# Performance work log

Hardware: AMD Instinct MI355X
Metric: run time of the kernel (lower is better)

The kernel has to match this reference:

```python
import jax, jax.numpy as jnp
import numpy as np

B, N = 1, 50000          # batch (module assumes 1), retrieval library size
VD, AD, OCRD, OD = 768, 768, 768, 384  # vision / audio / ocr / option dims
TOP_K = 25


def _l2norm(x):
    # torch.nn.functional.normalize(p=2, dim=-1) with eps=1e-12
    n = jnp.linalg.norm(x, axis=-1, keepdims=True)
    return x / jnp.maximum(n, 1e-12)


def setup_inputs() -> dict:
    key = jax.random.key(0)
    ks = jax.random.split(key, 8)
    return {
        "v":       jax.random.normal(ks[0], (B, VD), jnp.float32),
        "n_feats": jax.random.normal(ks[1], (B, N, VD), jnp.float32),
        "aud":     jax.random.normal(ks[2], (B, AD), jnp.float32),
        "n_auds":  jax.random.normal(ks[3], (B, N, AD), jnp.float32),
        "ocr":     jax.random.uniform(ks[4], (B, OCRD), jnp.float32),  # positive -> ocr.sum() > 0 branch
        "n_ocrs":  jax.random.normal(ks[5], (B, N, OCRD), jnp.float32),
        "o":       jax.random.normal(ks[6], (B, 3, OD), jnp.float32),
        "n_answ":  jax.random.normal(ks[7], (B, N, OD), jnp.float32),
        # learned temperature params (init zeros, as in torch)
        "temp_vid": jnp.zeros((1,), jnp.float32),
        "temp_aud": jnp.zeros((1,), jnp.float32),
        "temp_ocr": jnp.zeros((1,), jnp.float32),
    }


def _modal_attn(q, k):
    # normalized cosine scores, clipped to [0,1], then softmax over library dim
    s = jnp.einsum("bd,bnd->bn", _l2norm(q), _l2norm(k))
    return jax.nn.softmax(jnp.clip(s, 0.0, 1.0), axis=-1)


def reference(v, n_feats, aud, n_auds, ocr, n_ocrs, o, n_answ,
              temp_vid, temp_aud, temp_ocr):
    # gates (note: aud/ocr gates are multiplied by 0 exactly as in the source)
    vid_gate = jax.nn.sigmoid(temp_vid) * 2.0
    aud_gate = jax.nn.sigmoid(temp_aud) * 0.0
    ocr_gate = jax.nn.sigmoid(temp_ocr) * 0.0

    attention = (_modal_attn(v, n_feats) * vid_gate
                 + _modal_attn(aud, n_auds) * aud_gate
                 + _modal_attn(ocr, n_ocrs) * ocr_gate)  # [B, N]

    # TopKGroup (skip_self=False): keep only top-k entries via scatter mask
    _, idx = jax.lax.top_k(attention, TOP_K)            # [B, K]
    mask = jnp.zeros((attention.shape[-1],), attention.dtype).at[idx[0]].set(1.0)
    attention = attention * mask[None, :]

    # weighted sum of candidate answer embeddings, then dot with 3 options
    oia = jnp.einsum("bn,bnd->bd", attention, n_answ)   # [B, OD]
    scores = jnp.einsum("bd,bkd->bk", oia, o)           # [B, 3]
    return scores
```

## Files before the change

kernel.cpp:

```cpp
#include <hip/hip_runtime.h>
#include <cstdint>
#include <cstddef>

typedef unsigned long long u64;
typedef unsigned int u32;

constexpr int N    = 50000;
constexpr int D    = 768;
constexpr int OD   = 384;
constexpr int TOPK = 25;

constexpr int K1_BLOCKS  = 2048;
constexpr int K1_THREADS = 256;
constexpr int WAVES_TOTAL = K1_BLOCKS * (K1_THREADS / 64);

constexpr int N4    = 12500;
constexpr int BURST = 12;
constexpr int TAIL4 = N4 - BURST * 1024;
constexpr int CAP   = 4096;

constexpr int BINSHIFT = 20;

__global__ __launch_bounds__(K1_THREADS)
void k_scores(const float* __restrict__ v,
              const float* __restrict__ n_feats,
              float* __restrict__ s_out,
              float* __restrict__ part_out)
{
    const int lane  = threadIdx.x & 63;
    const int wib   = threadIdx.x >> 6;
    const int gwave = blockIdx.x * 4 + wib;

    const float4* v4 = reinterpret_cast<const float4*>(v);
    const float4 va = v4[lane];
    const float4 vb = v4[lane + 64];
    const float4 vc = v4[lane + 128];

    float vsq = 0.f;
    vsq = fmaf(va.x, va.x, vsq); vsq = fmaf(va.y, va.y, vsq);
    vsq = fmaf(va.z, va.z, vsq); vsq = fmaf(va.w, va.w, vsq);
    vsq = fmaf(vb.x, vb.x, vsq); vsq = fmaf(vb.y, vb.y, vsq);
    vsq = fmaf(vb.z, vb.z, vsq); vsq = fmaf(vb.w, vb.w, vsq);
    vsq = fmaf(vc.x, vc.x, vsq); vsq = fmaf(vc.y, vc.y, vsq);
    vsq = fmaf(vc.w, vc.w, vsq); vsq = fmaf(vc.z, vc.z, vsq);
    #pragma unroll
    for (int off = 32; off; off >>= 1) vsq += __shfl_xor(vsq, off);
    const float inv_vn = 1.0f / fmaxf(sqrtf(vsq), 1e-12f);

    float esum = 0.f;
    for (int r = 2 * gwave; r < N; r += 2 * WAVES_TOTAL) {
        const float4* f0 = reinterpret_cast<const float4*>(n_feats + (size_t)r * D);
        const float4* f1 = reinterpret_cast<const float4*>(n_feats + (size_t)(r + 1) * D);
        const float4 a0 = f0[lane];
        const float4 a1 = f0[lane + 64];
        const float4 a2 = f0[lane + 128];
        const float4 b0 = f1[lane];
        const float4 b1 = f1[lane + 64];
        const float4 b2 = f1[lane + 128];

        float dA = 0.f, nA = 0.f, dB = 0.f, nB = 0.f;
        dA = fmaf(a0.x, va.x, dA); nA = fmaf(a0.x, a0.x, nA);
        dB = fmaf(b0.x, va.x, dB); nB = fmaf(b0.x, b0.x, nB);
        dA = fmaf(a0.y, va.y, dA); nA = fmaf(a0.y, a0.y, nA);
        dB = fmaf(b0.y, va.y, dB); nB = fmaf(b0.y, b0.y, nB);
        dA = fmaf(a0.z, va.z, dA); nA = fmaf(a0.z, a0.z, nA);
        dB = fmaf(b0.z, va.z, dB); nB = fmaf(b0.z, b0.z, nB);
        dA = fmaf(a0.w, va.w, dA); nA = fmaf(a0.w, a0.w, nA);
        dB = fmaf(b0.w, va.w, dB); nB = fmaf(b0.w, b0.w, nB);
        dA = fmaf(a1.x, vb.x, dA); nA = fmaf(a1.x, a1.x, nA);
        dB = fmaf(b1.x, vb.x, dB); nB = fmaf(b1.x, b1.x, nB);
        dA = fmaf(a1.y, vb.y, dA); nA = fmaf(a1.y, a1.y, nA);
        dB = fmaf(b1.y, vb.y, dB); nB = fmaf(b1.y, b1.y, nB);
        dA = fmaf(a1.z, vb.z, dA); nA = fmaf(a1.z, a1.z, nA);
        dB = fmaf(b1.z, vb.z, dB); nB = fmaf(b1.z, b1.z, nB);
        dA = fmaf(a1.w, vb.w, dA); nA = fmaf(a1.w, a1.w, nA);
        dB = fmaf(b1.w, vb.w, dB); nB = fmaf(b1.w, b1.w, nB);
        dA = fmaf(a2.x, vc.x, dA); nA = fmaf(a2.x, a2.x, nA);
        dB = fmaf(b2.x, vc.x, dB); nB = fmaf(b2.x, b2.x, nB);
        dA = fmaf(a2.y, vc.y, dA); nA = fmaf(a2.y, a2.y, nA);
        dB = fmaf(b2.y, vc.y, dB); nB = fmaf(b2.y, b2.y, nB);
        dA = fmaf(a2.z, vc.z, dA); nA = fmaf(a2.z, a2.z, nA);
        dB = fmaf(b2.z, vc.z, dB); nB = fmaf(b2.z, b2.z, nB);
        dA = fmaf(a2.w, vc.w, dA); nA = fmaf(a2.w, a2.w, nA);
        dB = fmaf(b2.w, vc.w, dB); nB = fmaf(b2.w, b2.w, nB);

        #pragma unroll
        for (int off = 32; off; off >>= 1) {
            dA += __shfl_xor(dA, off);
            nA += __shfl_xor(nA, off);
            dB += __shfl_xor(dB, off);
            nB += __shfl_xor(nB, off);
        }

        float sA = dA * inv_vn / fmaxf(sqrtf(nA), 1e-12f);
        sA = fminf(fmaxf(sA, 0.f), 1.f);
        float sB = dB * inv_vn / fmaxf(sqrtf(nB), 1e-12f);
        sB = fminf(fmaxf(sB, 0.f), 1.f);
        if (lane == 0) {
            float2 sv; sv.x = sA; sv.y = sB;
            *reinterpret_cast<float2*>(s_out + r) = sv;
        }
        esum += expf(sA) + expf(sB);
    }

    __shared__ float wsum[4];
    if (lane == 0) wsum[wib] = esum;
    __syncthreads();
    if (threadIdx.x == 0)
        part_out[blockIdx.x] = (wsum[0] + wsum[1]) + (wsum[2] + wsum[3]);
}

__global__ __launch_bounds__(1024)
void k_finish(const float4* __restrict__ s4,
              const float* __restrict__ part,
              const float* __restrict__ n_answ,
              const float* __restrict__ o,
              const float* __restrict__ temp_vid,
              float* __restrict__ out)
{
    __shared__ u32   hist[1024];
    __shared__ u32   sufb[1024];
    __shared__ float redA[1024], redB[1024], redC[1024];
    __shared__ u64   L[CAP];
    __shared__ u64   Ls[TOPK];
    __shared__ float topw[TOPK];
    __shared__ int   topi[TOPK];
    __shared__ u32   ctrL;
    __shared__ int   b1sh;
    __shared__ float zsh;

    const int tid = threadIdx.x;

    redA[tid] = part[tid] + part[tid + 1024];
    hist[tid] = 0;
    if (tid == 0) { ctrL = 0; b1sh = 0; }
    __syncthreads();
    for (int s = 512; s > 0; s >>= 1) {
        if (tid < s) redA[tid] += redA[tid + s];
        __syncthreads();
    }
    if (tid == 0) zsh = redA[0];

    {
        float4 r[BURST];
        #pragma unroll
        for (int j = 0; j < BURST; ++j) r[j] = s4[tid + j * 1024];
        float4 rt;
        if (tid < TAIL4) rt = s4[BURST * 1024 + tid];

        #pragma unroll
        for (int j = 0; j < BURST; ++j) {
            u32 b;
            b = __float_as_uint(r[j].x); if (b) atomicAdd(&hist[b >> BINSHIFT], 1u);
            b = __float_as_uint(r[j].y); if (b) atomicAdd(&hist[b >> BINSHIFT], 1u);
            b = __float_as_uint(r[j].z); if (b) atomicAdd(&hist[b >> BINSHIFT], 1u);
            b = __float_as_uint(r[j].w); if (b) atomicAdd(&hist[b >> BINSHIFT], 1u);
        }
        if (tid < TAIL4) {
            u32 b;
            b = __float_as_uint(rt.x); if (b) atomicAdd(&hist[b >> BINSHIFT], 1u);
            b = __float_as_uint(rt.y); if (b) atomicAdd(&hist[b >> BINSHIFT], 1u);
            b = __float_as_uint(rt.z); if (b) atomicAdd(&hist[b >> BINSHIFT], 1u);
            b = __float_as_uint(rt.w); if (b) atomicAdd(&hist[b >> BINSHIFT], 1u);
        }
    }
    __syncthreads();

    {
        u32* src = hist;
        u32* dst = sufb;
        for (int s = 1; s < 1024; s <<= 1) {
            dst[tid] = src[tid] + ((tid + s < 1024) ? src[tid + s] : 0u);
            __syncthreads();
            u32* t_ = src; src = dst; dst = t_;
        }
        if (src[tid] >= (u32)TOPK && (tid == 1023 || src[tid + 1] < (u32)TOPK))
            b1sh = tid;
    }
    __syncthreads();
    const int b1 = b1sh;

    {
        float4 r[BURST];
        #pragma unroll
        for (int j = 0; j < BURST; ++j) r[j] = s4[tid + j * 1024];
        float4 rt;
        if (tid < TAIL4) rt = s4[BURST * 1024 + tid];

        #pragma unroll
        for (int j = 0; j < BURST; ++j) {
            const int base = (tid + j * 1024) * 4;
            u32 b;
            b = __float_as_uint(r[j].x);
            if (b && (int)(b >> BINSHIFT) >= b1) { u32 p = atomicAdd(&ctrL, 1u); if (p < CAP) L[p] = ((u64)b << 32) | (u64)(0xFFFFFFFFu - (u32)(base + 0)); }
            b = __float_as_uint(r[j].y);
            if (b && (int)(b >> BINSHIFT) >= b1) { u32 p = atomicAdd(&ctrL, 1u); if (p < CAP) L[p] = ((u64)b << 32) | (u64)(0xFFFFFFFFu - (u32)(base + 1)); }
            b = __float_as_uint(r[j].z);
            if (b && (int)(b >> BINSHIFT) >= b1) { u32 p = atomicAdd(&ctrL, 1u); if (p < CAP) L[p] = ((u64)b << 32) | (u64)(0xFFFFFFFFu - (u32)(base + 2)); }
            b = __float_as_uint(r[j].w);
            if (b && (int)(b >> BINSHIFT) >= b1) { u32 p = atomicAdd(&ctrL, 1u); if (p < CAP) L[p] = ((u64)b << 32) | (u64)(0xFFFFFFFFu - (u32)(base + 3)); }
        }
        if (tid < TAIL4) {
            const int base = (BURST * 1024 + tid) * 4;
            u32 b;
            b = __float_as_uint(rt.x);
            if (b && (int)(b >> BINSHIFT) >= b1) { u32 p = atomicAdd(&ctrL, 1u); if (p < CAP) L[p] = ((u64)b << 32) | (u64)(0xFFFFFFFFu - (u32)(base + 0)); }
            b = __float_as_uint(rt.y);
            if (b && (int)(b >> BINSHIFT) >= b1) { u32 p = atomicAdd(&ctrL, 1u); if (p < CAP) L[p] = ((u64)b << 32) | (u64)(0xFFFFFFFFu - (u32)(base + 1)); }
            b = __float_as_uint(rt.z);
            if (b && (int)(b >> BINSHIFT) >= b1) { u32 p = atomicAdd(&ctrL, 1u); if (p < CAP) L[p] = ((u64)b << 32) | (u64)(0xFFFFFFFFu - (u32)(base + 2)); }
            b = __float_as_uint(rt.w);
            if (b && (int)(b >> BINSHIFT) >= b1) { u32 p = atomicAdd(&ctrL, 1u); if (p < CAP) L[p] = ((u64)b << 32) | (u64)(0xFFFFFFFFu - (u32)(base + 3)); }
        }
    }
    __syncthreads();

    const int nL = (int)((ctrL < (u32)CAP) ? ctrL : (u32)CAP);
    for (int i = tid; i < nL; i += 1024) {
        const u64 ki = L[i];
        int rank = 0;
        for (int j = 0; j < nL; ++j) rank += (L[j] > ki);
        if (rank < TOPK) Ls[rank] = ki;
    }
    __syncthreads();

    if (tid < TOPK) {
        const u64 kk = Ls[tid];
        topw[tid] = expf(__uint_as_float((u32)(kk >> 32)));
        topi[tid] = (int)(0xFFFFFFFFu - (u32)(kk & 0xFFFFFFFFu));
    }
    __syncthreads();

    const float gate  = 2.f / (1.f + expf(-temp_vid[0]));
    const float scale = gate / zsh;
    float oia_ = 0.f;
    if (tid < OD) {
        #pragma unroll
        for (int j = 0; j < TOPK; ++j)
            oia_ = fmaf(topw[j] * scale, n_answ[(size_t)topi[j] * OD + tid], oia_);
    }
    redA[tid] = (tid < OD) ? oia_ * o[0 * OD + tid] : 0.f;
    redB[tid] = (tid < OD) ? oia_ * o[1 * OD + tid] : 0.f;
    redC[tid] = (tid < OD) ? oia_ * o[2 * OD + tid] : 0.f;
    __syncthreads();
    for (int s = 512; s > 0; s >>= 1) {
        if (tid < s) {
            redA[tid] += redA[tid + s];
            redB[tid] += redB[tid + s];
            redC[tid] += redC[tid + s];
        }
        __syncthreads();
    }
    if (tid == 0) { out[0] = redA[0]; out[1] = redB[0]; out[2] = redC[0]; }
}

extern "C" void kernel_launch(void* const* d_in, const int* in_sizes, int n_in,
                              void* d_out, int out_size, void* d_ws, size_t ws_size,
                              hipStream_t stream)
{
    const float* v        = (const float*)d_in[0];
    const float* n_feats  = (const float*)d_in[1];
    const float* o        = (const float*)d_in[6];
    const float* n_answ   = (const float*)d_in[7];
    const float* temp_vid = (const float*)d_in[8];
    float* out = (float*)d_out;

    char* ws = (char*)d_ws;
    float* ws_s    = (float*)(ws);
    float* ws_part = (float*)(ws + 200704);

    k_scores<<<K1_BLOCKS, K1_THREADS, 0, stream>>>(v, n_feats, ws_s, ws_part);
    k_finish<<<1, 1024, 0, stream>>>((const float4*)ws_s, ws_part, n_answ, o,
                                     temp_vid, out);
}
```

Measured before the change: 41.76 us.

## Build score histogram in scoring kernel and load scores once in finish

The score kernel now builds a per-block shared-memory histogram of score bit patterns and merges it into a global histogram with atomics. The finish kernel therefore no longer needs its own histogram pass over all 50000 scores, and it reads the scores into registers only once instead of twice. The top-k writes now go straight to the weight and index arrays, which removes one barrier. The costs are an extra memset launch, a global-atomic merge at the end of each of the 2048 blocks, and shared atomics done only by lane 0 inside the scoring loop.

```diff
diff --git a/kernel.cpp b/kernel.cpp
--- a/kernel.cpp
+++ b/kernel.cpp
@@ -25,11 +25,16 @@
 void k_scores(const float* __restrict__ v,
               const float* __restrict__ n_feats,
               float* __restrict__ s_out,
-              float* __restrict__ part_out)
+              float* __restrict__ part_out,
+              u32*   __restrict__ ghist)
 {
     const int lane  = threadIdx.x & 63;
     const int wib   = threadIdx.x >> 6;
     const int gwave = blockIdx.x * 4 + wib;
+
+    __shared__ u32 bhist[1024];
+    for (int i = threadIdx.x; i < 1024; i += K1_THREADS) bhist[i] = 0u;
+    __syncthreads();
 
     const float4* v4 = reinterpret_cast<const float4*>(v);
     const float4 va = v4[lane];
@@ -42,7 +47,7 @@
     vsq = fmaf(vb.x, vb.x, vsq); vsq = fmaf(vb.y, vb.y, vsq);
     vsq = fmaf(vb.z, vb.z, vsq); vsq = fmaf(vb.w, vb.w, vsq);
     vsq = fmaf(vc.x, vc.x, vsq); vsq = fmaf(vc.y, vc.y, vsq);
-    vsq = fmaf(vc.w, vc.w, vsq); vsq = fmaf(vc.z, vc.z, vsq);
+    vsq = fmaf(vc.z, vc.z, vsq); vsq = fmaf(vc.w, vc.w, vsq);
     #pragma unroll
     for (int off = 32; off; off >>= 1) vsq += __shfl_xor(vsq, off);
     const float inv_vn = 1.0f / fmaxf(sqrtf(vsq), 1e-12f);
@@ -99,6 +104,10 @@
         if (lane == 0) {
             float2 sv; sv.x = sA; sv.y = sB;
             *reinterpret_cast<float2*>(s_out + r) = sv;
+            const u32 ba = __float_as_uint(sA);
+            const u32 bb = __float_as_uint(sB);
+            if (ba) atomicAdd(&bhist[ba >> BINSHIFT], 1u);
+            if (bb) atomicAdd(&bhist[bb >> BINSHIFT], 1u);
         }
         esum += expf(sA) + expf(sB);
     }
@@ -108,21 +117,26 @@
     __syncthreads();
     if (threadIdx.x == 0)
         part_out[blockIdx.x] = (wsum[0] + wsum[1]) + (wsum[2] + wsum[3]);
+
+    for (int i = threadIdx.x; i < 1024; i += K1_THREADS) {
+        const u32 c = bhist[i];
+        if (c) atomicAdd(&ghist[i], c);
+    }
 }
 
 __global__ __launch_bounds__(1024)
 void k_finish(const float4* __restrict__ s4,
               const float* __restrict__ part,
+              const u32*  __restrict__ ghist,
               const float* __restrict__ n_answ,
               const float* __restrict__ o,
               const float* __restrict__ temp_vid,
               float* __restrict__ out)
 {
-    __shared__ u32   hist[1024];
-    __shared__ u32   sufb[1024];
+    __shared__ u32   hh[1024];
+    __shared__ u32   ss[1024];
     __shared__ float redA[1024], redB[1024], redC[1024];
     __shared__ u64   L[CAP];
-    __shared__ u64   Ls[TOPK];
     __shared__ float topw[TOPK];
     __shared__ int   topi[TOPK];
     __shared__ u32   ctrL;
@@ -131,8 +145,14 @@
 
     const int tid = threadIdx.x;
 
+    float4 r[BURST];
+    #pragma unroll
+    for (int j = 0; j < BURST; ++j) r[j] = s4[tid + j * 1024];
+    float4 rt = make_float4(0.f, 0.f, 0.f, 0.f);
+    if (tid < TAIL4) rt = s4[BURST * 1024 + tid];
+
+    hh[tid]   = ghist[tid];
     redA[tid] = part[tid] + part[tid + 1024];
-    hist[tid] = 0;
     if (tid == 0) { ctrL = 0; b1sh = 0; }
     __syncthreads();
     for (int s = 512; s > 0; s >>= 1) {
@@ -142,35 +162,10 @@
     if (tid == 0) zsh = redA[0];
 
     {
-        float4 r[BURST];
-        #pragma unroll
-        for (int j = 0; j < BURST; ++j) r[j] = s4[tid + j * 1024];
-        float4 rt;
-        if (tid < TAIL4) rt = s4[BURST * 1024 + tid];
-
-        #pragma unroll
-        for (int j = 0; j < BURST; ++j) {
-            u32 b;
-            b = __float_as_uint(r[j].x); if (b) atomicAdd(&hist[b >> BINSHIFT], 1u);
-            b = __float_as_uint(r[j].y); if (b) atomicAdd(&hist[b >> BINSHIFT], 1u);
-            b = __float_as_uint(r[j].z); if (b) atomicAdd(&hist[b >> BINSHIFT], 1u);
-            b = __float_as_uint(r[j].w); if (b) atomicAdd(&hist[b >> BINSHIFT], 1u);
-        }
-        if (tid < TAIL4) {
-            u32 b;
-            b = __float_as_uint(rt.x); if (b) atomicAdd(&hist[b >> BINSHIFT], 1u);
-            b = __float_as_uint(rt.y); if (b) atomicAdd(&hist[b >> BINSHIFT], 1u);
-            b = __float_as_uint(rt.z); if (b) atomicAdd(&hist[b >> BINSHIFT], 1u);
-            b = __float_as_uint(rt.w); if (b) atomicAdd(&hist[b >> BINSHIFT], 1u);
-        }
-    }
-    __syncthreads();
-
-    {
-        u32* src = hist;
-        u32* dst = sufb;
-        for (int s = 1; s < 1024; s <<= 1) {
-            dst[tid] = src[tid] + ((tid + s < 1024) ? src[tid + s] : 0u);
+        u32* src = hh;
+        u32* dst = ss;
+        for (int st = 1; st < 1024; st <<= 1) {
+            dst[tid] = src[tid] + ((tid + st < 1024) ? src[tid + st] : 0u);
             __syncthreads();
             u32* t_ = src; src = dst; dst = t_;
         }
@@ -180,54 +175,39 @@
     __syncthreads();
     const int b1 = b1sh;
 
-    {
-        float4 r[BURST];
-        #pragma unroll
-        for (int j = 0; j < BURST; ++j) r[j] = s4[tid + j * 1024];
-        float4 rt;
-        if (tid < TAIL4) rt = s4[BURST * 1024 + tid];
-
-        #pragma unroll
-        for (int j = 0; j < BURST; ++j) {
-            const int base = (tid + j * 1024) * 4;
-            u32 b;
-            b = __float_as_uint(r[j].x);
-            if (b && (int)(b >> BINSHIFT) >= b1) { u32 p = atomicAdd(&ctrL, 1u); if (p < CAP) L[p] = ((u64)b << 32) | (u64)(0xFFFFFFFFu - (u32)(base + 0)); }
-            b = __float_as_uint(r[j].y);
-            if (b && (int)(b >> BINSHIFT) >= b1) { u32 p = atomicAdd(&ctrL, 1u); if (p < CAP) L[p] = ((u64)b << 32) | (u64)(0xFFFFFFFFu - (u32)(base + 1)); }
-            b = __float_as_uint(r[j].z);
-            if (b && (int)(b >> BINSHIFT) >= b1) { u32 p = atomicAdd(&ctrL, 1u); if (p < CAP) L[p] = ((u64)b << 32) | (u64)(0xFFFFFFFFu - (u32)(base + 2)); }
-            b = __float_as_uint(r[j].w);
-            if (b && (int)(b >> BINSHIFT) >= b1) { u32 p = atomicAdd(&ctrL, 1u); if (p < CAP) L[p] = ((u64)b << 32) | (u64)(0xFFFFFFFFu - (u32)(base + 3)); }
-        }
-        if (tid < TAIL4) {
-            const int base = (BURST * 1024 + tid) * 4;
-            u32 b;
-            b = __float_as_uint(rt.x);
-            if (b && (int)(b >> BINSHIFT) >= b1) { u32 p = atomicAdd(&ctrL, 1u); if (p < CAP) L[p] = ((u64)b << 32) | (u64)(0xFFFFFFFFu - (u32)(base + 0)); }
-            b = __float_as_uint(rt.y);
-            if (b && (int)(b >> BINSHIFT) >= b1) { u32 p = atomicAdd(&ctrL, 1u); if (p < CAP) L[p] = ((u64)b << 32) | (u64)(0xFFFFFFFFu - (u32)(base + 1)); }
-            b = __float_as_uint(rt.z);
-            if (b && (int)(b >> BINSHIFT) >= b1) { u32 p = atomicAdd(&ctrL, 1u); if (p < CAP) L[p] = ((u64)b << 32) | (u64)(0xFFFFFFFFu - (u32)(base + 2)); }
-            b = __float_as_uint(rt.w);
-            if (b && (int)(b >> BINSHIFT) >= b1) { u32 p = atomicAdd(&ctrL, 1u); if (p < CAP) L[p] = ((u64)b << 32) | (u64)(0xFFFFFFFFu - (u32)(base + 3)); }
-        }
+    auto append = [&](u32 b, int e) {
+        if (b && (int)(b >> BINSHIFT) >= b1) {
+            const u32 p = atomicAdd(&ctrL, 1u);
+            if (p < (u32)CAP)
+                L[p] = ((u64)b << 32) | (u64)(0xFFFFFFFFu - (u32)e);
+        }
+    };
+    #pragma unroll
+    for (int j = 0; j < BURST; ++j) {
+        const int e = (tid + j * 1024) * 4;
+        append(__float_as_uint(r[j].x), e + 0);
+        append(__float_as_uint(r[j].y), e + 1);
+        append(__float_as_uint(r[j].z), e + 2);
+        append(__float_as_uint(r[j].w), e + 3);
+    }
+    if (tid < TAIL4) {
+        const int e = (BURST * 1024 + tid) * 4;
+        append(__float_as_uint(rt.x), e + 0);
+        append(__float_as_uint(rt.y), e + 1);
+        append(__float_as_uint(rt.z), e + 2);
+        append(__float_as_uint(rt.w), e + 3);
     }
     __syncthreads();
 
     const int nL = (int)((ctrL < (u32)CAP) ? ctrL : (u32)CAP);
     for (int i = tid; i < nL; i += 1024) {
         const u64 ki = L[i];
-        int rank = 0;
-        for (int j = 0; j < nL; ++j) rank += (L[j] > ki);
-        if (rank < TOPK) Ls[rank] = ki;
-    }
-    __syncthreads();
-
-    if (tid < TOPK) {
-        const u64 kk = Ls[tid];
-        topw[tid] = expf(__uint_as_float((u32)(kk >> 32)));
-        topi[tid] = (int)(0xFFFFFFFFu - (u32)(kk & 0xFFFFFFFFu));
+        int rk = 0;
+        for (int j = 0; j < nL; ++j) rk += (L[j] > ki);
+        if (rk < TOPK) {
+            topw[rk] = expf(__uint_as_float((u32)(ki >> 32)));
+            topi[rk] = (int)(0xFFFFFFFFu - (u32)(ki & 0xFFFFFFFFu));
+        }
     }
     __syncthreads();
 
@@ -239,8 +219,8 @@
         for (int j = 0; j < TOPK; ++j)
             oia_ = fmaf(topw[j] * scale, n_answ[(size_t)topi[j] * OD + tid], oia_);
     }
-    redA[tid] = (tid < OD) ? oia_ * o[0 * OD + tid] : 0.f;
-    redB[tid] = (tid < OD) ? oia_ * o[1 * OD + tid] : 0.f;
+    redA[tid] = (tid < OD) ? oia_ * o[tid]          : 0.f;
+    redB[tid] = (tid < OD) ? oia_ * o[OD + tid]     : 0.f;
     redC[tid] = (tid < OD) ? oia_ * o[2 * OD + tid] : 0.f;
     __syncthreads();
     for (int s = 512; s > 0; s >>= 1) {
@@ -268,8 +248,11 @@
     char* ws = (char*)d_ws;
     float* ws_s    = (float*)(ws);
     float* ws_part = (float*)(ws + 200704);
-
-    k_scores<<<K1_BLOCKS, K1_THREADS, 0, stream>>>(v, n_feats, ws_s, ws_part);
-    k_finish<<<1, 1024, 0, stream>>>((const float4*)ws_s, ws_part, n_answ, o,
-                                     temp_vid, out);
+    u32*   ws_hist = (u32*)  (ws + 208896);
+
+    hipMemsetAsync(ws_hist, 0, 4096, stream);
+    k_scores<<<K1_BLOCKS, K1_THREADS, 0, stream>>>(v, n_feats, ws_s, ws_part,
+                                                   ws_hist);
+    k_finish<<<1, 1024, 0, stream>>>((const float4*)ws_s, ws_part, ws_hist,
+                                     n_answ, o, temp_vid, out);
 }
```

Measured after the change: 56.46 us. +35.2%, slower.
